# Kernel tuning notes

Hardware: AMD Instinct MI355X
Metric: run time of the kernel (lower is better)

The kernel has to match this reference:

```python
import jax, jax.numpy as jnp
import numpy as np

BITS = 4
GROUP = 128
IN_F = 4096
OUT_F = 4096
N_TOK = 8192
N_STAGES = 4
QMAX = 2 ** BITS - 1  # affine (sym=False)


def _round_ste(x):
    return x + jax.lax.stop_gradient(jnp.round(x) - x)


def _clamp_ste(x, lo, hi):
    return x + jax.lax.stop_gradient(jnp.clip(x, lo, hi) - x)


def apply_rotation(x, pairs, theta, group_size):
    # x: [N, H]; pairs: [R, H] int (per-group index pairs in [0, group_size));
    # theta: [R, H//2]
    n, h = x.shape
    g = h // group_size
    half = group_size // 2
    offsets = (jnp.arange(g, dtype=jnp.int32) * group_size)[:, None]  # [G,1]
    pair_view = pairs.reshape(pairs.shape[0], g, half, 2)
    theta_view = theta.reshape(theta.shape[0], g, half)
    out = x
    for r in range(pairs.shape[0]):  # small fixed number of rotation stages
        idx_i = (pair_view[r, :, :, 0] + offsets).reshape(-1)  # [H//2]
        idx_j = (pair_view[r, :, :, 1] + offsets).reshape(-1)
        xi = out[:, idx_i]  # [N, H//2]
        xj = out[:, idx_j]
        c = jnp.cos(theta_view[r]).reshape(-1)[None, :]
        s = jnp.sin(theta_view[r]).reshape(-1)[None, :]
        out = out.at[:, idx_i].set(xi * c + xj * s).at[:, idx_j].set(-xi * s + xj * c)
    return out


def quant_dequant_affine_ste(w, scale, zero_point_float, group_size):
    # pseudo_quantize_dequant with sym=False, use_ste=True
    view = w.reshape(-1, group_size)
    s = _clamp_ste(scale, 1e-5, 1e5)
    rzp = _clamp_ste(-_round_ste(zero_point_float), 0.0, float(QMAX))
    q = _round_ste(view / s) + rzp
    q = _clamp_ste(q, 0.0, float(QMAX))
    return ((q - rzp) * s).reshape(w.shape)


def setup_inputs() -> dict:
    key = jax.random.key(0)
    k1, k2, k3, k4 = jax.random.split(key, 4)
    x = jax.random.normal(k1, (N_TOK, IN_F), dtype=jnp.float32)
    weight = jax.random.normal(k2, (OUT_F, IN_F), dtype=jnp.float32) * 0.02
    bias = jax.random.normal(k3, (OUT_F,), dtype=jnp.float32) * 0.01
    channel_scales = jnp.ones((IN_F,), dtype=jnp.float32)
    theta = jax.random.normal(k4, (N_STAGES, IN_F // 2), dtype=jnp.float32) * 0.05
    # per-group pair permutations: each stage/group is a permutation of [0, GROUP)
    rng = np.random.default_rng(0)
    g = IN_F // GROUP
    pairs_np = np.stack([
        np.concatenate([rng.permutation(GROUP) for _ in range(g)])
        for _ in range(N_STAGES)
    ]).astype(np.int32)  # [R, IN_F]
    pairs = jnp.asarray(pairs_np)
    # affine qparams from initial (theta=0, scales=1) transformed weight == weight
    view = weight.reshape(-1, GROUP)
    min_val = view.min(axis=1, keepdims=True)
    max_val = view.max(axis=1, keepdims=True)
    q_scale = jnp.clip(max_val - min_val, 1e-5, None) / QMAX
    q_zero_point = min_val / q_scale
    theta_mask = jnp.ones((N_STAGES, IN_F // 2), dtype=bool)
    return {"x": x, "weight": weight, "bias": bias,
            "channel_scales": channel_scales, "theta": theta,
            "q_scale": q_scale, "q_zero_point": q_zero_point,
            "pairs": pairs, "theta_mask": theta_mask}


def reference(x, weight, bias, channel_scales, theta, q_scale, q_zero_point, pairs, theta_mask):
    # transformed_weight(): scale input channels then group-wise Givens rotate
    w_scaled = weight * channel_scales[None, :]
    w_t = apply_rotation(w_scaled, pairs, theta, GROUP)
    # STE pseudo quantize-dequantize in the transformed domain
    w_q = quant_dequant_affine_ste(w_t, q_scale, q_zero_point, GROUP)
    # inverse rotation back to the original input domain, undo channel scales
    w_back = apply_rotation(w_q, pairs[::-1], -theta[::-1], GROUP) / channel_scales[None, :]
    return x @ w_back.T + bias[None, :]
```

## Files before the change

### kernel.cpp

```cpp
#include <hip/hip_runtime.h>
#include <hip/hip_bf16.h>
#include <math.h>

#define IN_F    4096
#define OUT_F   4096
#define N_TOK   8192
#define GROUP   128
#define NSTAGE  4
#define NPAIRS  2048
#define QMAXF   15.0
#define ROWS_PW 8

typedef unsigned short u16;
typedef __bf16 bf16x8 __attribute__((ext_vector_type(8)));
typedef float  f32x4  __attribute__((ext_vector_type(4)));

struct alignas(8) U16x4 { u16 x, y, z, w; };

__device__ __forceinline__ u16 f2bf(float f) {
    unsigned u = __float_as_uint(f);
    unsigned r = (u + 0x7fffu + ((u >> 16) & 1u)) >> 16;
    return (u16)r;
}

__device__ __forceinline__ void gl_lds16(const void* g, void* l) {
    __builtin_amdgcn_global_load_lds(
        (const __attribute__((address_space(1))) void*)g,
        (__attribute__((address_space(3))) void*)l,
        16, 0, 0);
}

__global__ void make_tabs(const float* __restrict__ theta,
                          double* __restrict__ ctab, double* __restrict__ stab) {
    int i = blockIdx.x * 256 + threadIdx.x;
    if (i < NSTAGE * NPAIRS) {
        double t = (double)theta[i];
        ctab[i] = cos(t);
        stab[i] = sin(t);
    }
}

__global__ __launch_bounds__(256) void build_w(
    const float* __restrict__ weight, const float* __restrict__ cs,
    const float* __restrict__ qs, const float* __restrict__ qzp,
    const int* __restrict__ pairs,
    const double* __restrict__ ctab, const double* __restrict__ stab,
    u16* __restrict__ wb) {
    __shared__ double gbuf[4][GROUP];
    const int wave = threadIdx.x >> 6, l = threadIdx.x & 63;
    const int task = blockIdx.x * 4 + wave;
    const int ob = task >> 5, g = task & 31;
    const int o0 = ob * ROWS_PW;
    double* gb = gbuf[wave];
    const int e0 = g * GROUP;

    const int2* prs = (const int2*)pairs;
    int2   pr_[NSTAGE];
    double c_[NSTAGE], s_[NSTAGE];
#pragma unroll
    for (int r = 0; r < NSTAGE; ++r) {
        pr_[r] = prs[r * (IN_F / 2) + g * 64 + l];
        c_[r]  = ctab[r * NPAIRS + g * 64 + l];
        s_[r]  = stab[r * NPAIRS + g * 64 + l];
    }
    float2 cv = *(const float2*)(cs + e0 + 2 * l);
    const double cvx = (double)cv.x, cvy = (double)cv.y;
    const double rcx = 1.0 / cvx, rcy = 1.0 / cvy;

    for (int o = o0; o < o0 + ROWS_PW; ++o) {
        float2 wv = *(const float2*)(weight + (size_t)o * IN_F + e0 + 2 * l);
        gb[2 * l]     = (double)wv.x * cvx;
        gb[2 * l + 1] = (double)wv.y * cvy;
        __builtin_amdgcn_wave_barrier();

#pragma unroll
        for (int r = 0; r < NSTAGE; ++r) {
            double xi = gb[pr_[r].x], xj = gb[pr_[r].y];
            __builtin_amdgcn_wave_barrier();
            gb[pr_[r].x] =  xi * c_[r] + xj * s_[r];
            gb[pr_[r].y] = -xi * s_[r] + xj * c_[r];
            __builtin_amdgcn_wave_barrier();
        }

        {
            double sc  = fmin(fmax((double)qs[o * 32 + g], 1e-5), 1e5);
            double rzp = fmin(fmax(-rint((double)qzp[o * 32 + g]), 0.0), QMAXF);
            double inv = 1.0 / sc;
#pragma unroll
            for (int e = 2 * l; e <= 2 * l + 1; ++e) {
                double q = rint(gb[e] * inv) + rzp;
                q = fmin(fmax(q, 0.0), QMAXF);
                gb[e] = (q - rzp) * sc;
            }
            __builtin_amdgcn_wave_barrier();
        }

#pragma unroll
        for (int r = NSTAGE - 1; r >= 0; --r) {
            double xi = gb[pr_[r].x], xj = gb[pr_[r].y];
            __builtin_amdgcn_wave_barrier();
            gb[pr_[r].x] = xi * c_[r] - xj * s_[r];
            gb[pr_[r].y] = xi * s_[r] + xj * c_[r];
            __builtin_amdgcn_wave_barrier();
        }

        unsigned lo = f2bf((float)(gb[2 * l]     * rcx));
        unsigned hi = f2bf((float)(gb[2 * l + 1] * rcy));
        *(unsigned*)(wb + (size_t)o * IN_F + e0 + 2 * l) = lo | (hi << 16);
        __builtin_amdgcn_wave_barrier();
    }
}

__global__ void cast_x(const float* __restrict__ x, u16* __restrict__ xb) {
    size_t i = ((size_t)blockIdx.x * 256 + threadIdx.x) * 4;
    float4 v = *(const float4*)(x + i);
    U16x4 o;
    o.x = f2bf(v.x); o.y = f2bf(v.y); o.z = f2bf(v.z); o.w = f2bf(v.w);
    *(U16x4*)(xb + i) = o;
}

__global__ __launch_bounds__(512, 2) void gemm_bt(
    const u16* __restrict__ A, const u16* __restrict__ B,
    const float* __restrict__ bias, float* __restrict__ C) {
    constexpr int K = IN_F;
    constexpr int N = OUT_F;
    constexpr int NS = K / 32;
    __shared__ __align__(16) u16 As[4][256 * 32];
    __shared__ __align__(16) u16 Bs[4][256 * 32];

    const int tid  = threadIdx.x;
    const int wave = tid >> 6, lane = tid & 63;
    const int lrow = lane & 15, lq = lane >> 4;
    const int wm = wave >> 2, wn = wave & 3;

    const int wg = (blockIdx.x & 7) * 64 + (blockIdx.x >> 3);
    const int mt = wg & 31, nt = wg >> 5;
    const int m0 = mt * 256, n0 = nt * 256;

    const int srow = tid >> 2;
    const int gch  = (tid & 3) ^ ((tid >> 3) & 3);
    const u16* pA0 = A + (size_t)(m0 + srow) * K + gch * 8;
    const u16* pA1 = pA0 + (size_t)128 * K;
    const u16* pB0 = B + (size_t)(n0 + srow) * K + gch * 8;
    const u16* pB1 = pB0 + (size_t)128 * K;

#define STAGE(slot, s) do {                                         \
        const int ko_ = (s) * 32;                                   \
        gl_lds16(pA0 + ko_, &As[slot][wave * 512]);                 \
        gl_lds16(pA1 + ko_, &As[slot][4096 + wave * 512]);          \
        gl_lds16(pB0 + ko_, &Bs[slot][wave * 512]);                 \
        gl_lds16(pB1 + ko_, &Bs[slot][4096 + wave * 512]);          \
    } while (0)

    f32x4 acc[8][4];
#pragma unroll
    for (int i = 0; i < 8; ++i)
#pragma unroll
        for (int j = 0; j < 4; ++j) acc[i][j] = (f32x4){0.f, 0.f, 0.f, 0.f};

    STAGE(0, 0); STAGE(1, 1); STAGE(2, 2);

#define BODY(s, VMSTR, DO_STAGE) do {                                          \
        asm volatile("s_waitcnt " VMSTR);                                      \
        __builtin_amdgcn_s_barrier();                                          \
        asm volatile("" ::: "memory");                                         \
        const u16* as_ = As[(s) & 3];                                          \
        const u16* bs_ = Bs[(s) & 3];                                          \
        bf16x8 af[8], bf[4];                                                   \
        _Pragma("unroll")                                                      \
        for (int mi = 0; mi < 8; ++mi) {                                       \
            int ar = wm * 128 + mi * 16 + lrow;                                \
            af[mi] = *(const bf16x8*)&as_[ar * 32 +                            \
                                          (((lq ^ (ar >> 1)) & 3) << 3)];      \
        }                                                                      \
        _Pragma("unroll")                                                      \
        for (int nj = 0; nj < 4; ++nj) {                                       \
            int br = wn * 64 + nj * 16 + lrow;                                 \
            bf[nj] = *(const bf16x8*)&bs_[br * 32 +                            \
                                          (((lq ^ (br >> 1)) & 3) << 3)];      \
        }                                                                      \
        if (DO_STAGE) STAGE(((s) + 3) & 3, (s) + 3);                           \
        __builtin_amdgcn_s_setprio(1);                                         \
        _Pragma("unroll")                                                      \
        for (int mi = 0; mi < 8; ++mi)                                         \
            _Pragma("unroll")                                                  \
            for (int nj = 0; nj < 4; ++nj)                                     \
                acc[mi][nj] = __builtin_amdgcn_mfma_f32_16x16x32_bf16(         \
                    af[mi], bf[nj], acc[mi][nj], 0, 0, 0);                     \
        __builtin_amdgcn_s_setprio(0);                                         \
        asm volatile("" ::: "memory");                                         \
    } while (0)

    for (int s = 0; s < NS - 3; ++s)
        BODY(s, "vmcnt(8)", 1);
    BODY(NS - 3, "vmcnt(8)", 0);
    BODY(NS - 2, "vmcnt(4)", 0);
    BODY(NS - 1, "vmcnt(0)", 0);

#undef BODY
#undef STAGE

#pragma unroll
    for (int mi = 0; mi < 8; ++mi) {
        int rb = m0 + wm * 128 + mi * 16 + lq * 4;
#pragma unroll
        for (int nj = 0; nj < 4; ++nj) {
            int col = n0 + wn * 64 + nj * 16 + lrow;
            float bv = bias[col];
#pragma unroll
            for (int r = 0; r < 4; ++r)
                C[(size_t)(rb + r) * N + col] = acc[mi][nj][r] + bv;
        }
    }
}

extern "C" void kernel_launch(void* const* d_in, const int* in_sizes, int n_in,
                              void* d_out, int out_size, void* d_ws, size_t ws_size,
                              hipStream_t stream) {
    const float* x    = (const float*)d_in[0];
    const float* w    = (const float*)d_in[1];
    const float* bias = (const float*)d_in[2];
    const float* cs   = (const float*)d_in[3];
    const float* th   = (const float*)d_in[4];
    const float* qs   = (const float*)d_in[5];
    const float* qzp  = (const float*)d_in[6];
    const int*   pr   = (const int*)d_in[7];
    float* out = (float*)d_out;

    char* ws = (char*)d_ws;
    double* ctab = (double*)ws;
    double* stab = (double*)(ws + 65536);
    u16*    xb   = (u16*)(ws + 131072);
    u16*    wb   = (u16*)(ws + 131072 + (size_t)N_TOK * IN_F * 2);

    hipLaunchKernelGGL(make_tabs, dim3((NSTAGE * NPAIRS + 255) / 256), dim3(256),
                       0, stream, th, ctab, stab);
    hipLaunchKernelGGL(build_w, dim3(OUT_F / ROWS_PW * 32 / 4), dim3(256),
                       0, stream, w, cs, qs, qzp, pr, ctab, stab, wb);
    hipLaunchKernelGGL(cast_x, dim3(N_TOK * IN_F / 4 / 256), dim3(256), 0, stream,
                       x, xb);
    hipLaunchKernelGGL(gemm_bt, dim3((N_TOK / 256) * (OUT_F / 256)), dim3(512),
                       0, stream, xb, wb, bias, out);
}
```

Baseline: 615.2 us.

## Replace LDS-based Givens rotation stages with register permutes via ds_bpermute

The weight-transform kernel now keeps each lane's pair of values in registers and moves them between stages with precomputed cross-lane permutation descriptors using ds_bpermute, instead of scattering and gathering doubles through shared memory. The permutation tables are built once per wave before the row loop. This is meant to remove the LDS round-trips and wave barriers around every rotation stage. In exchange, each stage costs several 32-bit bpermutes per double. The gain only touches build_w, which is likely a small part of a run dominated by the GEMM.

Result: slower. 642.9 us (+4.5%).

```diff
diff --git a/kernel.cpp b/kernel.cpp
--- a/kernel.cpp
+++ b/kernel.cpp
@@ -30,6 +30,20 @@
         16, 0, 0);
 }
 
+__device__ __forceinline__ double bperm64(int addr, double v) {
+    long long u = __double_as_longlong(v);
+    int lo = __builtin_amdgcn_ds_bpermute(addr, (int)u);
+    int hi = __builtin_amdgcn_ds_bpermute(addr, (int)(u >> 32));
+    return __longlong_as_double(((long long)(unsigned)lo) |
+                                ((long long)hi << 32));
+}
+__device__ __forceinline__ double fetch2(double a, double b, int desc) {
+    int addr = (desc >> 1) << 2;
+    double va = bperm64(addr, a);
+    double vb = bperm64(addr, b);
+    return (desc & 1) ? vb : va;
+}
+
 __global__ void make_tabs(const float* __restrict__ theta,
                           double* __restrict__ ctab, double* __restrict__ stab) {
     int i = blockIdx.x * 256 + threadIdx.x;
@@ -46,69 +60,98 @@
     const int* __restrict__ pairs,
     const double* __restrict__ ctab, const double* __restrict__ stab,
     u16* __restrict__ wb) {
-    __shared__ double gbuf[4][GROUP];
+    __shared__ int ptab[4][128];
     const int wave = threadIdx.x >> 6, l = threadIdx.x & 63;
     const int task = blockIdx.x * 4 + wave;
     const int ob = task >> 5, g = task & 31;
     const int o0 = ob * ROWS_PW;
-    double* gb = gbuf[wave];
+    int* pt = ptab[wave];
     const int e0 = g * GROUP;
 
     const int2* prs = (const int2*)pairs;
-    int2   pr_[NSTAGE];
+    int2   pp[NSTAGE];
     double c_[NSTAGE], s_[NSTAGE];
 #pragma unroll
     for (int r = 0; r < NSTAGE; ++r) {
-        pr_[r] = prs[r * (IN_F / 2) + g * 64 + l];
-        c_[r]  = ctab[r * NPAIRS + g * 64 + l];
-        s_[r]  = stab[r * NPAIRS + g * 64 + l];
+        pp[r] = prs[r * (IN_F / 2) + g * 64 + l];
+        c_[r] = ctab[r * NPAIRS + g * 64 + l];
+        s_[r] = stab[r * NPAIRS + g * 64 + l];
     }
     float2 cv = *(const float2*)(cs + e0 + 2 * l);
     const double cvx = (double)cv.x, cvy = (double)cv.y;
     const double rcx = 1.0 / cvx, rcy = 1.0 / cvy;
 
+    int t1x, t1y, toutx, touty;
+    int t2x, t2y, it0x, it0y;
+    int t3x, t3y, it1x, it1y;
+    int it2x, it2y;
+    pt[pp[0].x] = l << 1; pt[pp[0].y] = (l << 1) | 1;
+    __builtin_amdgcn_wave_barrier();
+    t1x = pt[pp[1].x]; t1y = pt[pp[1].y];
+    toutx = pt[2 * l]; touty = pt[2 * l + 1];
+    __builtin_amdgcn_wave_barrier();
+    pt[pp[1].x] = l << 1; pt[pp[1].y] = (l << 1) | 1;
+    __builtin_amdgcn_wave_barrier();
+    t2x = pt[pp[2].x]; t2y = pt[pp[2].y];
+    it0x = pt[pp[0].x]; it0y = pt[pp[0].y];
+    __builtin_amdgcn_wave_barrier();
+    pt[pp[2].x] = l << 1; pt[pp[2].y] = (l << 1) | 1;
+    __builtin_amdgcn_wave_barrier();
+    t3x = pt[pp[3].x]; t3y = pt[pp[3].y];
+    it1x = pt[pp[1].x]; it1y = pt[pp[1].y];
+    __builtin_amdgcn_wave_barrier();
+    pt[pp[3].x] = l << 1; pt[pp[3].y] = (l << 1) | 1;
+    __builtin_amdgcn_wave_barrier();
+    it2x = pt[pp[2].x]; it2y = pt[pp[2].y];
+
+#define TRANS(dx, dy) do {                                                     \
+        double nx_ = fetch2(xi, xj, dx);                                       \
+        double ny_ = fetch2(xi, xj, dy);                                       \
+        xi = nx_; xj = ny_;                                                    \
+    } while (0)
+#define ROT_F(r) do {                                                          \
+        double t_ = xi * c_[r] + xj * s_[r];                                   \
+        xj = -xi * s_[r] + xj * c_[r];                                         \
+        xi = t_;                                                               \
+    } while (0)
+#define ROT_I(r) do {                                                          \
+        double t_ = xi * c_[r] - xj * s_[r];                                   \
+        xj = xi * s_[r] + xj * c_[r];                                          \
+        xi = t_;                                                               \
+    } while (0)
+
     for (int o = o0; o < o0 + ROWS_PW; ++o) {
         float2 wv = *(const float2*)(weight + (size_t)o * IN_F + e0 + 2 * l);
-        gb[2 * l]     = (double)wv.x * cvx;
-        gb[2 * l + 1] = (double)wv.y * cvy;
-        __builtin_amdgcn_wave_barrier();
-
-#pragma unroll
-        for (int r = 0; r < NSTAGE; ++r) {
-            double xi = gb[pr_[r].x], xj = gb[pr_[r].y];
-            __builtin_amdgcn_wave_barrier();
-            gb[pr_[r].x] =  xi * c_[r] + xj * s_[r];
-            gb[pr_[r].y] = -xi * s_[r] + xj * c_[r];
-            __builtin_amdgcn_wave_barrier();
-        }
+        double v0 = (double)wv.x * cvx;
+        double v1 = (double)wv.y * cvy;
+        double xi = fetch2(v0, v1, pp[0].x);
+        double xj = fetch2(v0, v1, pp[0].y);
+        ROT_F(0);
+        TRANS(t1x, t1y); ROT_F(1);
+        TRANS(t2x, t2y); ROT_F(2);
+        TRANS(t3x, t3y); ROT_F(3);
 
         {
             double sc  = fmin(fmax((double)qs[o * 32 + g], 1e-5), 1e5);
             double rzp = fmin(fmax(-rint((double)qzp[o * 32 + g]), 0.0), QMAXF);
             double inv = 1.0 / sc;
-#pragma unroll
-            for (int e = 2 * l; e <= 2 * l + 1; ++e) {
-                double q = rint(gb[e] * inv) + rzp;
-                q = fmin(fmax(q, 0.0), QMAXF);
-                gb[e] = (q - rzp) * sc;
-            }
-            __builtin_amdgcn_wave_barrier();
+            xi = (fmin(fmax(rint(xi * inv) + rzp, 0.0), QMAXF) - rzp) * sc;
+            xj = (fmin(fmax(rint(xj * inv) + rzp, 0.0), QMAXF) - rzp) * sc;
         }
 
-#pragma unroll
-        for (int r = NSTAGE - 1; r >= 0; --r) {
-            double xi = gb[pr_[r].x], xj = gb[pr_[r].y];
-            __builtin_amdgcn_wave_barrier();
-            gb[pr_[r].x] = xi * c_[r] - xj * s_[r];
-            gb[pr_[r].y] = xi * s_[r] + xj * c_[r];
-            __builtin_amdgcn_wave_barrier();
-        }
-
-        unsigned lo = f2bf((float)(gb[2 * l]     * rcx));
-        unsigned hi = f2bf((float)(gb[2 * l + 1] * rcy));
+        ROT_I(3);
+        TRANS(it2x, it2y); ROT_I(2);
+        TRANS(it1x, it1y); ROT_I(1);
+        TRANS(it0x, it0y); ROT_I(0);
+        double r0 = fetch2(xi, xj, toutx);
+        double r1 = fetch2(xi, xj, touty);
+        unsigned lo = f2bf((float)(r0 * rcx));
+        unsigned hi = f2bf((float)(r1 * rcy));
         *(unsigned*)(wb + (size_t)o * IN_F + e0 + 2 * l) = lo | (hi << 16);
-        __builtin_amdgcn_wave_barrier();
-    }
+    }
+#undef TRANS
+#undef ROT_F
+#undef ROT_I
 }
 
 __global__ void cast_x(const float* __restrict__ x, u16* __restrict__ xb) {
```

## Restructure GEMM main loop into 64-wide K double-buffer with split-phase staging

Applied to the files above, without the earlier changes.

The bf16 GEMM main loop moves from a 4-slot ring of 32-wide K stages to a 2-slot double buffer of 64-wide K tiles. Each tile is processed in four phases of 16 MFMAs, separated by barriers, with A and B half-tile loads interleaved between phases and explicit vmcnt waits. The intent is to overlap global-to-LDS loads with MFMA work more finely and to reuse A fragments across two B pairs, while precomputing the LDS swizzle once. The cost is more barriers per K step, and the hand-tuned waitcnt sequence carries a correctness risk.

New measurement: 709.5 us. 15.3% more time.

```diff
diff --git a/kernel.cpp b/kernel.cpp
--- a/kernel.cpp
+++ b/kernel.cpp
@@ -124,14 +124,15 @@
     const float* __restrict__ bias, float* __restrict__ C) {
     constexpr int K = IN_F;
     constexpr int N = OUT_F;
-    constexpr int NS = K / 32;
-    __shared__ __align__(16) u16 As[4][256 * 32];
-    __shared__ __align__(16) u16 Bs[4][256 * 32];
+    constexpr int NT = K / 64;
+    __shared__ __align__(16) u16 As[2][2][256 * 32];
+    __shared__ __align__(16) u16 Bs[2][2][256 * 32];
 
     const int tid  = threadIdx.x;
     const int wave = tid >> 6, lane = tid & 63;
     const int lrow = lane & 15, lq = lane >> 4;
     const int wm = wave >> 2, wn = wave & 3;
+    const int swz = (lq ^ ((lrow >> 1) & 3)) << 3;
 
     const int wg = (blockIdx.x & 7) * 64 + (blockIdx.x >> 3);
     const int mt = wg & 31, nt = wg >> 5;
@@ -139,66 +140,107 @@
 
     const int srow = tid >> 2;
     const int gch  = (tid & 3) ^ ((tid >> 3) & 3);
-    const u16* pA0 = A + (size_t)(m0 + srow) * K + gch * 8;
-    const u16* pA1 = pA0 + (size_t)128 * K;
-    const u16* pB0 = B + (size_t)(n0 + srow) * K + gch * 8;
-    const u16* pB1 = pB0 + (size_t)128 * K;
-
-#define STAGE(slot, s) do {                                         \
-        const int ko_ = (s) * 32;                                   \
-        gl_lds16(pA0 + ko_, &As[slot][wave * 512]);                 \
-        gl_lds16(pA1 + ko_, &As[slot][4096 + wave * 512]);          \
-        gl_lds16(pB0 + ko_, &Bs[slot][wave * 512]);                 \
-        gl_lds16(pB1 + ko_, &Bs[slot][4096 + wave * 512]);          \
-    } while (0)
-
-    f32x4 acc[8][4];
-#pragma unroll
-    for (int i = 0; i < 8; ++i)
-#pragma unroll
-        for (int j = 0; j < 4; ++j) acc[i][j] = (f32x4){0.f, 0.f, 0.f, 0.f};
-
-    STAGE(0, 0); STAGE(1, 1); STAGE(2, 2);
-
-#define BODY(s, VMSTR, DO_STAGE) do {                                          \
-        asm volatile("s_waitcnt " VMSTR);                                      \
-        __builtin_amdgcn_s_barrier();                                          \
-        asm volatile("" ::: "memory");                                         \
-        const u16* as_ = As[(s) & 3];                                          \
-        const u16* bs_ = Bs[(s) & 3];                                          \
-        bf16x8 af[8], bf[4];                                                   \
+    const u16* pA = A + (size_t)(m0 + srow) * K + gch * 8;
+    const u16* pB = B + (size_t)(n0 + srow) * K + gch * 8;
+
+#define STG_A(slot, t, h) do {                                                 \
+        gl_lds16(pA + (t) * 64 + (h) * 32, &As[slot][h][wave << 9]);           \
+        gl_lds16(pA + (size_t)128 * K + (t) * 64 + (h) * 32,                   \
+                 &As[slot][h][4096 + (wave << 9)]);                            \
+    } while (0)
+#define STG_B(slot, t, h) do {                                                 \
+        gl_lds16(pB + (t) * 64 + (h) * 32, &Bs[slot][h][wave << 9]);           \
+        gl_lds16(pB + (size_t)128 * K + (t) * 64 + (h) * 32,                   \
+                 &Bs[slot][h][4096 + (wave << 9)]);                            \
+    } while (0)
+
+#define RD_A(dst, asp) do {                                                    \
         _Pragma("unroll")                                                      \
-        for (int mi = 0; mi < 8; ++mi) {                                       \
-            int ar = wm * 128 + mi * 16 + lrow;                                \
-            af[mi] = *(const bf16x8*)&as_[ar * 32 +                            \
-                                          (((lq ^ (ar >> 1)) & 3) << 3)];      \
+        for (int mi_ = 0; mi_ < 8; ++mi_) {                                    \
+            const int ar_ = (wm << 7) + (mi_ << 4) + lrow;                     \
+            dst[mi_] = *(const bf16x8*)&(asp)[ar_ * 32 + swz];                 \
         }                                                                      \
-        _Pragma("unroll")                                                      \
-        for (int nj = 0; nj < 4; ++nj) {                                       \
-            int br = wn * 64 + nj * 16 + lrow;                                 \
-            bf[nj] = *(const bf16x8*)&bs_[br * 32 +                            \
-                                          (((lq ^ (br >> 1)) & 3) << 3)];      \
-        }                                                                      \
-        if (DO_STAGE) STAGE(((s) + 3) & 3, (s) + 3);                           \
+    } while (0)
+#define RD_B(bsp, nj) (*(const bf16x8*)&(bsp)[((wn << 6) + ((nj) << 4) + lrow) * 32 + swz])
+
+#define MFQ(av, bx, by, c0, c1) do {                                           \
         __builtin_amdgcn_s_setprio(1);                                         \
         _Pragma("unroll")                                                      \
-        for (int mi = 0; mi < 8; ++mi)                                         \
-            _Pragma("unroll")                                                  \
-            for (int nj = 0; nj < 4; ++nj)                                     \
-                acc[mi][nj] = __builtin_amdgcn_mfma_f32_16x16x32_bf16(         \
-                    af[mi], bf[nj], acc[mi][nj], 0, 0, 0);                     \
+        for (int mi_ = 0; mi_ < 8; ++mi_) {                                    \
+            acc[mi_][c0] = __builtin_amdgcn_mfma_f32_16x16x32_bf16(            \
+                av[mi_], bx, acc[mi_][c0], 0, 0, 0);                           \
+            acc[mi_][c1] = __builtin_amdgcn_mfma_f32_16x16x32_bf16(            \
+                av[mi_], by, acc[mi_][c1], 0, 0, 0);                           \
+        }                                                                      \
         __builtin_amdgcn_s_setprio(0);                                         \
-        asm volatile("" ::: "memory");                                         \
-    } while (0)
-
-    for (int s = 0; s < NS - 3; ++s)
-        BODY(s, "vmcnt(8)", 1);
-    BODY(NS - 3, "vmcnt(8)", 0);
-    BODY(NS - 2, "vmcnt(4)", 0);
-    BODY(NS - 1, "vmcnt(0)", 0);
-
-#undef BODY
-#undef STAGE
+    } while (0)
+
+#define BAR1() do { asm volatile("" ::: "memory");                             \
+        __builtin_amdgcn_s_barrier();                                          \
+        asm volatile("s_waitcnt lgkmcnt(0)" ::: "memory"); } while (0)
+#define BAR2() do { asm volatile("" ::: "memory");                             \
+        __builtin_amdgcn_s_barrier();                                          \
+        asm volatile("" ::: "memory"); } while (0)
+
+    f32x4 acc[8][4];
+#pragma unroll
+    for (int i = 0; i < 8; ++i)
+#pragma unroll
+        for (int j = 0; j < 4; ++j) acc[i][j] = (f32x4){0.f, 0.f, 0.f, 0.f};
+
+    STG_A(0, 0, 0); STG_B(0, 0, 0);
+    STG_A(0, 0, 1); STG_B(0, 0, 1);
+    STG_A(1, 1, 0);
+    asm volatile("s_waitcnt vmcnt(6)" ::: "memory");
+    __builtin_amdgcn_s_barrier();
+    asm volatile("" ::: "memory");
+
+    for (int u = 0; u < NT; ++u) {
+        const u16* as0 = &As[u & 1][0][0];
+        const u16* as1 = &As[u & 1][1][0];
+        const u16* bs0 = &Bs[u & 1][0][0];
+        const u16* bs1 = &Bs[u & 1][1][0];
+        const int sn = (u + 1) & 1;
+        bf16x8 a0[8], a1[8], b0, b1, b2, b3;
+
+        RD_A(a0, as0);
+        b0 = RD_B(bs0, 0); b1 = RD_B(bs0, 1);
+        if (u + 1 < NT) STG_B(sn, u + 1, 0);
+        BAR1();
+        MFQ(a0, b0, b1, 0, 1);
+        BAR2();
+
+        b2 = RD_B(bs0, 2); b3 = RD_B(bs0, 3);
+        if (u + 1 < NT) STG_A(sn, u + 1, 1);
+        if (u < NT - 1) asm volatile("s_waitcnt vmcnt(6)" ::: "memory");
+        else            asm volatile("s_waitcnt vmcnt(0)" ::: "memory");
+        BAR1();
+        MFQ(a0, b2, b3, 2, 3);
+        BAR2();
+
+        RD_A(a1, as1);
+        b0 = RD_B(bs1, 0); b1 = RD_B(bs1, 1);
+        if (u + 1 < NT) STG_B(sn, u + 1, 1);
+        BAR1();
+        MFQ(a1, b0, b1, 0, 1);
+        BAR2();
+
+        b2 = RD_B(bs1, 2); b3 = RD_B(bs1, 3);
+        if (u + 2 < NT) STG_A(u & 1, u + 2, 0);
+        if (u < NT - 2)       asm volatile("s_waitcnt vmcnt(6)" ::: "memory");
+        else if (u == NT - 2) asm volatile("s_waitcnt vmcnt(4)" ::: "memory");
+        BAR1();
+        MFQ(a1, b2, b3, 2, 3);
+        BAR2();
+    }
+
+#undef STG_A
+#undef STG_B
+#undef RD_A
+#undef RD_B
+#undef MFQ
+#undef BAR1
+#undef BAR2
 
 #pragma unroll
     for (int mi = 0; mi < 8; ++mi) {
```
